# Performance work log

Measured on AMD Instinct MI355X. Metric: run time of the kernel, lower is better.

The kernel has to match this reference:

```python
import jax, jax.numpy as jnp
import numpy as np

B, T, D, H = 8, 2048, 512, 128

def setup_inputs() -> dict:
    key = jax.random.key(0)
    ks = jax.random.split(key, 8)
    s = lambda fan_in: 1.0 / np.sqrt(fan_in)
    return {
        "x": jax.random.normal(ks[0], (B, T, D), jnp.float32),
        "prediction": jax.random.normal(ks[1], (B, T, D), jnp.float32),
        "Wq": jax.random.uniform(ks[2], (D, H), jnp.float32, -s(D), s(D)),
        "bq": jnp.zeros((H,), jnp.float32),
        "Wk": jax.random.uniform(ks[3], (D, H), jnp.float32, -s(D), s(D)),
        "bk": jnp.zeros((H,), jnp.float32),
        "Wv": jax.random.uniform(ks[4], (D, D), jnp.float32, -s(D), s(D)),
        "bv": jnp.zeros((D,), jnp.float32),
        "Wf": jax.random.uniform(ks[5], (2 * D, D), jnp.float32, -s(2 * D), s(2 * D)),
        "bf": jnp.zeros((D,), jnp.float32),
    }

def reference(x, prediction, Wq, bq, Wk, bk, Wv, bv, Wf, bf):
    # q,k: [B,T,H]; v: [B,T,D]
    q = jnp.einsum('btd,dh->bth', prediction, Wq) + bq
    k = jnp.einsum('btd,dh->bth', x, Wk) + bk
    v = jnp.einsum('btd,de->bte', x, Wv) + bv
    # unscaled attention scores [B,T,T]
    scores = jnp.einsum('bth,bsh->bts', q, k)
    attn = jax.nn.softmax(scores, axis=-1)
    attended = jnp.einsum('bts,bsd->btd', attn, v)
    fusion_input = jnp.concatenate([prediction, attended], axis=-1)  # [B,T,2D]
    return jax.nn.sigmoid(jnp.einsum('btf,fd->btd', fusion_input, Wf) + bf)
```

## Files before the change

kernel.cpp:

```cpp
#include <hip/hip_runtime.h>
#include <hip/hip_bf16.h>


#define APF_B 8
#define APF_T 2048
#define APF_D 512
#define APF_H 128
#define APF_M (APF_B * APF_T)
#define FA_SB 64

typedef unsigned short u16;
typedef __attribute__((ext_vector_type(8))) short short8;
typedef __attribute__((ext_vector_type(4))) float f32x4;
typedef __attribute__((ext_vector_type(16))) float f32x16;

static __device__ __forceinline__ u16 f2bf(float x) {
    union { float f; unsigned int u; } cv;
    cv.f = x;
    unsigned int u = cv.u + 0x7FFFu + ((cv.u >> 16) & 1u);
    return (u16)(u >> 16);
}

static __device__ __forceinline__ void load16_lds(const u16* g, u16* l) {
    __builtin_amdgcn_global_load_lds(
        (const __attribute__((address_space(1))) unsigned int*)g,
        (__attribute__((address_space(3))) unsigned int*)l,
        16, 0, 0);
}

static __device__ __forceinline__ f32x16 zero16() {
    f32x16 v;
#pragma unroll
    for (int i = 0; i < 16; ++i) v[i] = 0.f;
    return v;
}


__global__ __launch_bounds__(256) void prep_all(
    const float* __restrict__ x,    u16* __restrict__ xb,
    const float* __restrict__ pred, u16* __restrict__ predb, long n4,
    const float* __restrict__ Wq, u16* __restrict__ WqT,
    const float* __restrict__ Wk, u16* __restrict__ WkT,
    const float* __restrict__ Wv, u16* __restrict__ WvT,
    const float* __restrict__ Wf, u16* __restrict__ WfT)
{
    const int bid = blockIdx.x;
    if (bid < 1024) {
        long i = bid * 256L + threadIdx.x;
        const long stride = 1024 * 256L;
        for (; i < 2 * n4; i += stride) {
            const float* in = (i < n4) ? x : pred;
            u16* out = (i < n4) ? xb : predb;
            const long j = (i < n4) ? i : (i - n4);
            const float4 v = ((const float4*)in)[j];
            ushort4 o;
            o.x = f2bf(v.x); o.y = f2bf(v.y); o.z = f2bf(v.z); o.w = f2bf(v.w);
            ((ushort4*)out)[j] = o;
        }
    } else {
        const long e = (bid - 1024) * 256L + threadIdx.x;
        if (e < 65536) {
            const long idx = e;
            const long n = idx / 512, k = idx % 512;
            WqT[idx] = f2bf(Wq[k * 128 + n]);
        } else if (e < 131072) {
            const long idx = e - 65536;
            const long n = idx / 512, k = idx % 512;
            WkT[idx] = f2bf(Wk[k * 128 + n]);
        } else if (e < 393216) {
            const long idx = e - 131072;
            const long n = idx / 512, k = idx % 512;
            WvT[idx] = f2bf(Wv[k * 512 + n]);
        } else if (e < 917504) {
            const long idx = e - 393216;
            const long n = idx / 1024, k = idx % 1024;
            WfT[idx] = f2bf(Wf[k * 512 + n]);
        }
    }
}

template <int DUAL, int EPI, int BIASM, int VBLK>
__global__ __launch_bounds__(256) void mfma_gemm(
    const u16* __restrict__ Ap, const u16* __restrict__ A2p, long lda,
    const u16* __restrict__ Bp, const u16* __restrict__ Bp2, long ldb,
    const float* __restrict__ biasp, const float* __restrict__ bias2,
    void* __restrict__ Cp, void* __restrict__ Cp2, long ldc, int K,
    long sA, long sB, long sC)
{
    __shared__ u16 smA[2][128 * 32];
    __shared__ u16 smB[2][128 * 32];

    const int tid  = threadIdx.x;
    const int lane = tid & 63;
    const int wid  = tid >> 6;
    const int wr   = wid >> 1;
    const int wc   = wid & 1;

    const long row0 = (long)blockIdx.y * 128;
    const long col0 = (long)blockIdx.x * 128;
    const long z    = blockIdx.z;

    const u16* Abase = (DUAL == 2) ? (z ? A2p : Ap) : (Ap + z * sA);
    const u16* Bbase = (DUAL == 2) ? (z ? Bp2 : Bp) : (Bp + z * sB);

    f32x4 acc[4][4];
#pragma unroll
    for (int i = 0; i < 4; ++i)
#pragma unroll
        for (int j = 0; j < 4; ++j)
            acc[i][j] = (f32x4){0.f, 0.f, 0.f, 0.f};

    const int lrow = (lane >> 4) * 4;
    const int lcol = lane & 15;
    const int q8   = (lane >> 4) * 8;

    auto stage = [&](int buf, int kb) {
#pragma unroll
        for (int rep = 0; rep < 2; ++rep) {
            const int c  = tid + rep * 256;
            const int r  = c >> 2;
            const int kc = (c & 3) * 8;
            const int wbase = (wid * 64 + rep * 256) * 8;
            const u16* ga;
            if (DUAL == 1 && (kb + kc) >= APF_D) {
                ga = A2p + (row0 + r) * lda + (kb + kc - APF_D);
            } else {
                ga = Abase + (row0 + r) * lda + (kb + kc);
            }
            load16_lds(ga, &smA[buf][wbase]);
            const u16* gb = Bbase + (col0 + r) * ldb + (kb + kc);
            load16_lds(gb, &smB[buf][wbase]);
        }
    };

    const int NT = K / 32;
    stage(0, 0);
    __syncthreads();
    int cur = 0;

    for (int t = 0; t < NT; ++t) {
        if (t + 1 < NT) stage(cur ^ 1, (t + 1) * 32);

        short8 av[4], bv4[4];
#pragma unroll
        for (int ti = 0; ti < 4; ++ti)
            av[ti] = *(const short8*)&smA[cur][(wr * 64 + ti * 16 + lcol) * 32 + q8];
#pragma unroll
        for (int tj = 0; tj < 4; ++tj)
            bv4[tj] = *(const short8*)&smB[cur][(wc * 64 + tj * 16 + lcol) * 32 + q8];

#pragma unroll
        for (int ti = 0; ti < 4; ++ti)
#pragma unroll
            for (int tj = 0; tj < 4; ++tj)
                acc[ti][tj] = __builtin_amdgcn_mfma_f32_16x16x32_bf16(
                    av[ti], bv4[tj], acc[ti][tj], 0, 0, 0);

        __syncthreads();
        cur ^= 1;
    }

    const float* bias = (DUAL == 2 && z) ? bias2 : biasp;

#pragma unroll
    for (int ti = 0; ti < 4; ++ti) {
        const long m0t = row0 + wr * 64 + ti * 16 + lrow;
#pragma unroll
        for (int tj = 0; tj < 4; ++tj) {
            const long n = col0 + wc * 64 + tj * 16 + lcol;
            const float bn = (BIASM == 0 && bias != nullptr) ? bias[n] : 0.f;
            if (EPI == 0) {
                u16* C = (u16*)((DUAL == 2 && z) ? Cp2 : Cp) + ((DUAL == 2) ? 0 : z * sC);
#pragma unroll
                for (int r = 0; r < 4; ++r) {
                    const long m = m0t + r;
                    const float bm = (BIASM == 1) ? bias[m] : bn;
                    long idx;
                    if (VBLK) {
                        idx = ((((m >> 5) * 256) + (n >> 3)) << 8) +
                              ((m & 31) << 3) + (n & 7);
                    } else {
                        idx = m * ldc + n;
                    }
                    C[idx] = f2bf(acc[ti][tj][r] + bm);
                }
            } else {
                float* C = (float*)Cp;
#pragma unroll
                for (int r = 0; r < 4; ++r) {
                    const float val = acc[ti][tj][r] + bn;
                    C[(m0t + r) * ldc + n] = 1.0f / (1.0f + expf(-val));
                }
            }
        }
    }
}

__global__ __launch_bounds__(256, 3) void attn_fused(
    const u16* __restrict__ qg, const u16* __restrict__ kg,
    const u16* __restrict__ vTg, u16* __restrict__ attg)
{
    __shared__ u16 sQ[64 * 128];
    __shared__ u16 sK[64 * 128];
    __shared__ u16 sP[64 * 64];
    __shared__ float sRS[192];

    const int tid  = threadIdx.x;
    const int lane = tid & 63;
    const int w    = tid >> 6;
    const int l31  = lane & 31;
    const int hi   = lane >> 5;
    const int qb   = w >> 1;
    const int sb   = w & 1;

    const int  bid = blockIdx.x;
    const long z   = bid & 7;
    const int  r   = bid >> 3;
    const long q0  = (long)(r & 31) * 64;
    const long d0  = (long)(r >> 5) * 256;

    const u16* kbase0 = kg + z * (long)APF_T * APF_H;

    {
        const u16* qsrc = qg + (z * APF_T + q0) * APF_H;
#pragma unroll
        for (int rep = 0; rep < 4; ++rep) {
            const int c    = tid + rep * 256;
            const int row  = c >> 4;
            const int col8 = (c & 15) * 8;
            load16_lds(qsrc + row * APF_H + (col8 ^ ((row & 15) << 3)), &sQ[c * 8]);
        }
#pragma unroll
        for (int rep = 0; rep < 4; ++rep) {
            const int c    = tid + rep * 256;
            const int row  = c >> 4;
            const int col8 = (c & 15) * 8;
            load16_lds(kbase0 + row * APF_H + (col8 ^ ((row & 15) << 3)), &sK[c * 8]);
        }
    }
    __syncthreads();

    f32x16 oacc[2][2];
#pragma unroll
    for (int i = 0; i < 2; ++i)
#pragma unroll
        for (int j = 0; j < 2; ++j) oacc[i][j] = zero16();
    f32x16 rsacc = zero16();

    const long dblk0 = (d0 >> 5) + w * 2;
    const u16* vzb = vTg + z * 1048576L + dblk0 * 65536L + (long)l31 * 8;

    const int qrow = qb * 32 + l31;
    const int krow = sb * 32 + l31;
    const int pcol = sb * 32 + l31;

    for (int kt = 0; kt < APF_T / FA_SB; ++kt) {
        f32x16 sacc = zero16();
#pragma unroll
        for (int ks = 0; ks < 8; ++ks) {
            const int colk = ks * 16 + hi * 8;
            const short8 av = *(const short8*)&sQ[qrow * 128 + (colk ^ ((qrow & 15) << 3))];
            const short8 bv = *(const short8*)&sK[krow * 128 + (colk ^ ((krow & 15) << 3))];
            sacc = __builtin_amdgcn_mfma_f32_32x32x16_bf16(av, bv, sacc, 0, 0, 0);
        }
        __syncthreads();

        if (kt + 1 < APF_T / FA_SB) {
            const u16* ksrc = kbase0 + (long)(kt + 1) * FA_SB * APF_H;
#pragma unroll
            for (int rep = 0; rep < 4; ++rep) {
                const int c    = tid + rep * 256;
                const int row  = c >> 4;
                const int col8 = (c & 15) * 8;
                load16_lds(ksrc + row * APF_H + (col8 ^ ((row & 15) << 3)), &sK[c * 8]);
            }
        }

        const long sbase = (long)kt * 8 + hi;
        short8 vf1[2][2];
#pragma unroll
        for (int dt = 0; dt < 2; ++dt)
#pragma unroll
            for (int ks = 0; ks < 2; ++ks)
                vf1[dt][ks] = *(const short8*)(vzb + dt * 65536L + (sbase + ks * 2) * 256);

#pragma unroll
        for (int rg = 0; rg < 16; ++rg) {
            const float e = __expf(sacc[rg]);
            rsacc[rg] += e;
            const int prow = qb * 32 + (rg & 3) + 8 * (rg >> 2) + 4 * hi;
            sP[prow * 64 + (pcol ^ ((prow & 7) << 3))] = f2bf(e);
        }
        __syncthreads();

#pragma unroll
        for (int ks = 0; ks < 2; ++ks) {
            const int colk = ks * 16 + hi * 8;
            short8 pa[2];
#pragma unroll
            for (int qt = 0; qt < 2; ++qt) {
                const int prow = qt * 32 + l31;
                pa[qt] = *(const short8*)&sP[prow * 64 + (colk ^ ((prow & 7) << 3))];
            }
#pragma unroll
            for (int dt = 0; dt < 2; ++dt)
#pragma unroll
                for (int qt = 0; qt < 2; ++qt)
                    oacc[qt][dt] = __builtin_amdgcn_mfma_f32_32x32x16_bf16(
                        pa[qt], vf1[dt][ks], oacc[qt][dt], 0, 0, 0);
        }

        short8 vf2[2][2];
#pragma unroll
        for (int dt = 0; dt < 2; ++dt)
#pragma unroll
            for (int ks = 0; ks < 2; ++ks)
                vf2[dt][ks] = *(const short8*)(vzb + dt * 65536L + (sbase + (ks + 2) * 2) * 256);

#pragma unroll
        for (int ks = 0; ks < 2; ++ks) {
            const int colk = (ks + 2) * 16 + hi * 8;
            short8 pa[2];
#pragma unroll
            for (int qt = 0; qt < 2; ++qt) {
                const int prow = qt * 32 + l31;
                pa[qt] = *(const short8*)&sP[prow * 64 + (colk ^ ((prow & 7) << 3))];
            }
#pragma unroll
            for (int dt = 0; dt < 2; ++dt)
#pragma unroll
                for (int qt = 0; qt < 2; ++qt)
                    oacc[qt][dt] = __builtin_amdgcn_mfma_f32_32x32x16_bf16(
                        pa[qt], vf2[dt][ks], oacc[qt][dt], 0, 0, 0);
        }
    }

#pragma unroll
    for (int rg = 0; rg < 16; ++rg) {
        float s = rsacc[rg];
        s += __shfl_xor(s, 1);
        s += __shfl_xor(s, 2);
        s += __shfl_xor(s, 4);
        s += __shfl_xor(s, 8);
        s += __shfl_xor(s, 16);
        rsacc[rg] = s;
    }
    if (l31 == 0) {
#pragma unroll
        for (int rg = 0; rg < 16; ++rg) {
            const int row = (rg & 3) + 8 * (rg >> 2) + 4 * hi;
            sRS[w * 32 + row] = rsacc[rg];
        }
    }
    __syncthreads();
    if (tid < 64) {
        const int qb2 = tid >> 5, r2 = tid & 31;
        sRS[128 + tid] = 1.0f / (sRS[(qb2 * 2 + 0) * 32 + r2] +
                                 sRS[(qb2 * 2 + 1) * 32 + r2]);
    }
    __syncthreads();

    const long rowg0 = z * APF_T + q0;
    const long colg0 = d0 + (long)w * 64;
#pragma unroll
    for (int qt = 0; qt < 2; ++qt)
#pragma unroll
        for (int rg = 0; rg < 16; ++rg) {
            const int row = qt * 32 + (rg & 3) + 8 * (rg >> 2) + 4 * hi;
            const float inv = sRS[128 + row];
#pragma unroll
            for (int dt = 0; dt < 2; ++dt)
                attg[(rowg0 + row) * APF_D + colg0 + dt * 32 + l31] =
                    f2bf(oacc[qt][dt][rg] * inv);
        }
}

extern "C" void kernel_launch(void* const* d_in, const int* in_sizes, int n_in,
                              void* d_out, int out_size, void* d_ws, size_t ws_size,
                              hipStream_t stream)
{
    (void)in_sizes; (void)n_in; (void)out_size; (void)ws_size;

    const float* x    = (const float*)d_in[0];
    const float* pred = (const float*)d_in[1];
    const float* Wq   = (const float*)d_in[2];
    const float* bq   = (const float*)d_in[3];
    const float* Wk   = (const float*)d_in[4];
    const float* bk   = (const float*)d_in[5];
    const float* Wv   = (const float*)d_in[6];
    const float* bv   = (const float*)d_in[7];
    const float* Wf   = (const float*)d_in[8];
    const float* bfu  = (const float*)d_in[9];

    u16* wsp   = (u16*)d_ws;
    u16* xb    = wsp;
    u16* predb = xb    + (long)APF_M * APF_D;
    u16* qb    = predb + (long)APF_M * APF_D;
    u16* kbuf  = qb    + (long)APF_M * APF_H;
    u16* vTb   = kbuf  + (long)APF_M * APF_H;
    u16* attb  = vTb   + (long)APF_M * APF_D;
    u16* WqT   = attb  + (long)APF_M * APF_D;
    u16* WkT   = WqT   + (long)APF_H * APF_D;
    u16* WvT   = WkT   + (long)APF_H * APF_D;
    u16* WfT   = WvT   + (long)APF_D * APF_D;

    const dim3 thr(256);
    const long nBTD4 = (long)APF_M * APF_D / 4;

    prep_all<<<dim3(1024 + 3584), thr, 0, stream>>>(
        x, xb, pred, predb, nBTD4, Wq, WqT, Wk, WkT, Wv, WvT, Wf, WfT);

    mfma_gemm<2, 0, 0, 0><<<dim3(1, 128, 2), thr, 0, stream>>>(
        predb, xb, APF_D, WqT, WkT, APF_D, bq, bk, qb, kbuf, APF_H, APF_D,
        0, 0, 0);

    mfma_gemm<0, 0, 1, 1><<<dim3(16, 4, 8), thr, 0, stream>>>(
        WvT, nullptr, APF_D, xb, nullptr, APF_D, bv, nullptr, vTb, nullptr,
        APF_T, APF_D, 0, (long)APF_T * APF_D, (long)APF_D * APF_T);

    attn_fused<<<dim3(512), thr, 0, stream>>>(qb, kbuf, vTb, attb);

    mfma_gemm<1, 2, 0, 0><<<dim3(4, 128, 1), thr, 0, stream>>>(
        predb, attb, APF_D, WfT, nullptr, 2 * APF_D, bfu, nullptr, d_out, nullptr,
        APF_D, 2 * APF_D, 0, 0, 0);
}
```

Baseline: 262.7 us.

## Split attention output columns finer and keep Q fragments in registers

Each attention block now produces 128 output columns instead of 256, doubling the grid to 1024 blocks. Q fragments are loaded directly into registers instead of LDS, and each wave holds half the output accumulators. This aims to raise occupancy and fill more CUs, but it doubles the redundant QK^T score and exp computation across column splits.

```diff
diff --git a/kernel.cpp b/kernel.cpp
--- a/kernel.cpp
+++ b/kernel.cpp
@@ -200,7 +200,6 @@
     const u16* __restrict__ qg, const u16* __restrict__ kg,
     const u16* __restrict__ vTg, u16* __restrict__ attg)
 {
-    __shared__ u16 sQ[64 * 128];
     __shared__ u16 sK[64 * 128];
     __shared__ u16 sP[64 * 64];
     __shared__ float sRS[192];
@@ -217,40 +216,34 @@
     const long z   = bid & 7;
     const int  r   = bid >> 3;
     const long q0  = (long)(r & 31) * 64;
-    const long d0  = (long)(r >> 5) * 256;
+    const long d0  = (long)(r >> 5) * 128;
 
     const u16* kbase0 = kg + z * (long)APF_T * APF_H;
 
+#pragma unroll
+    for (int rep = 0; rep < 4; ++rep) {
+        const int c    = tid + rep * 256;
+        const int row  = c >> 4;
+        const int col8 = (c & 15) * 8;
+        load16_lds(kbase0 + row * APF_H + (col8 ^ ((row & 15) << 3)), &sK[c * 8]);
+    }
+
+    short8 qf[8];
     {
-        const u16* qsrc = qg + (z * APF_T + q0) * APF_H;
-#pragma unroll
-        for (int rep = 0; rep < 4; ++rep) {
-            const int c    = tid + rep * 256;
-            const int row  = c >> 4;
-            const int col8 = (c & 15) * 8;
-            load16_lds(qsrc + row * APF_H + (col8 ^ ((row & 15) << 3)), &sQ[c * 8]);
-        }
-#pragma unroll
-        for (int rep = 0; rep < 4; ++rep) {
-            const int c    = tid + rep * 256;
-            const int row  = c >> 4;
-            const int col8 = (c & 15) * 8;
-            load16_lds(kbase0 + row * APF_H + (col8 ^ ((row & 15) << 3)), &sK[c * 8]);
-        }
+        const u16* qsrc = qg + (z * APF_T + q0 + qb * 32 + l31) * APF_H;
+#pragma unroll
+        for (int ks = 0; ks < 8; ++ks)
+            qf[ks] = *(const short8*)(qsrc + ks * 16 + hi * 8);
     }
     __syncthreads();
 
-    f32x16 oacc[2][2];
-#pragma unroll
-    for (int i = 0; i < 2; ++i)
-#pragma unroll
-        for (int j = 0; j < 2; ++j) oacc[i][j] = zero16();
+    f32x16 oacc[2];
+    oacc[0] = zero16(); oacc[1] = zero16();
     f32x16 rsacc = zero16();
 
-    const long dblk0 = (d0 >> 5) + w * 2;
+    const long dblk0 = (d0 >> 5) + w;
     const u16* vzb = vTg + z * 1048576L + dblk0 * 65536L + (long)l31 * 8;
 
-    const int qrow = qb * 32 + l31;
     const int krow = sb * 32 + l31;
     const int pcol = sb * 32 + l31;
 
@@ -259,9 +252,8 @@
 #pragma unroll
         for (int ks = 0; ks < 8; ++ks) {
             const int colk = ks * 16 + hi * 8;
-            const short8 av = *(const short8*)&sQ[qrow * 128 + (colk ^ ((qrow & 15) << 3))];
             const short8 bv = *(const short8*)&sK[krow * 128 + (colk ^ ((krow & 15) << 3))];
-            sacc = __builtin_amdgcn_mfma_f32_32x32x16_bf16(av, bv, sacc, 0, 0, 0);
+            sacc = __builtin_amdgcn_mfma_f32_32x32x16_bf16(qf[ks], bv, sacc, 0, 0, 0);
         }
         __syncthreads();
 
@@ -277,12 +269,10 @@
         }
 
         const long sbase = (long)kt * 8 + hi;
-        short8 vf1[2][2];
-#pragma unroll
-        for (int dt = 0; dt < 2; ++dt)
-#pragma unroll
-            for (int ks = 0; ks < 2; ++ks)
-                vf1[dt][ks] = *(const short8*)(vzb + dt * 65536L + (sbase + ks * 2) * 256);
+        short8 vf[4];
+#pragma unroll
+        for (int ks = 0; ks < 4; ++ks)
+            vf[ks] = *(const short8*)(vzb + (sbase + ks * 2) * 256);
 
 #pragma unroll
         for (int rg = 0; rg < 16; ++rg) {
@@ -294,7 +284,7 @@
         __syncthreads();
 
 #pragma unroll
-        for (int ks = 0; ks < 2; ++ks) {
+        for (int ks = 0; ks < 4; ++ks) {
             const int colk = ks * 16 + hi * 8;
             short8 pa[2];
 #pragma unroll
@@ -303,35 +293,9 @@
                 pa[qt] = *(const short8*)&sP[prow * 64 + (colk ^ ((prow & 7) << 3))];
             }
 #pragma unroll
-            for (int dt = 0; dt < 2; ++dt)
-#pragma unroll
-                for (int qt = 0; qt < 2; ++qt)
-                    oacc[qt][dt] = __builtin_amdgcn_mfma_f32_32x32x16_bf16(
-                        pa[qt], vf1[dt][ks], oacc[qt][dt], 0, 0, 0);
-        }
-
-        short8 vf2[2][2];
-#pragma unroll
-        for (int dt = 0; dt < 2; ++dt)
-#pragma unroll
-            for (int ks = 0; ks < 2; ++ks)
-                vf2[dt][ks] = *(const short8*)(vzb + dt * 65536L + (sbase + (ks + 2) * 2) * 256);
-
-#pragma unroll
-        for (int ks = 0; ks < 2; ++ks) {
-            const int colk = (ks + 2) * 16 + hi * 8;
-            short8 pa[2];
-#pragma unroll
-            for (int qt = 0; qt < 2; ++qt) {
-                const int prow = qt * 32 + l31;
-                pa[qt] = *(const short8*)&sP[prow * 64 + (colk ^ ((prow & 7) << 3))];
-            }
-#pragma unroll
-            for (int dt = 0; dt < 2; ++dt)
-#pragma unroll
-                for (int qt = 0; qt < 2; ++qt)
-                    oacc[qt][dt] = __builtin_amdgcn_mfma_f32_32x32x16_bf16(
-                        pa[qt], vf2[dt][ks], oacc[qt][dt], 0, 0, 0);
+            for (int qt = 0; qt < 2; ++qt)
+                oacc[qt] = __builtin_amdgcn_mfma_f32_32x32x16_bf16(
+                    pa[qt], vf[ks], oacc[qt], 0, 0, 0);
         }
     }
 
@@ -361,17 +325,14 @@
     __syncthreads();
 
     const long rowg0 = z * APF_T + q0;
-    const long colg0 = d0 + (long)w * 64;
+    const long colg  = d0 + (long)w * 32 + l31;
 #pragma unroll
     for (int qt = 0; qt < 2; ++qt)
 #pragma unroll
         for (int rg = 0; rg < 16; ++rg) {
             const int row = qt * 32 + (rg & 3) + 8 * (rg >> 2) + 4 * hi;
-            const float inv = sRS[128 + row];
-#pragma unroll
-            for (int dt = 0; dt < 2; ++dt)
-                attg[(rowg0 + row) * APF_D + colg0 + dt * 32 + l31] =
-                    f2bf(oacc[qt][dt][rg] * inv);
+            attg[(rowg0 + row) * APF_D + colg] =
+                f2bf(oacc[qt][rg] * sRS[128 + row]);
         }
 }
 
@@ -418,7 +379,7 @@
         WvT, nullptr, APF_D, xb, nullptr, APF_D, bv, nullptr, vTb, nullptr,
         APF_T, APF_D, 0, (long)APF_T * APF_D, (long)APF_D * APF_T);
 
-    attn_fused<<<dim3(512), thr, 0, stream>>>(qb, kbuf, vTb, attb);
+    attn_fused<<<dim3(1024), thr, 0, stream>>>(qb, kbuf, vTb, attb);
 
     mfma_gemm<1, 2, 0, 0><<<dim3(4, 128, 1), thr, 0, stream>>>(
         predb, attb, APF_D, WfT, nullptr, 2 * APF_D, bfu, nullptr, d_out, nullptr,
```

After: 290.4 us. 10.6% more time.

## Fuse fp32-to-bf16 activation conversion into GEMM loaders and merge Q/K/V GEMMs

Applied to the files above, without the earlier changes.

The separate pass that converted x and prediction to bf16 is removed. GEMMs now load fp32 activations into registers, convert them and write bf16 into LDS, while weights still arrive through direct-to-LDS DMA. The Q/K and V projection GEMMs are merged into one launch, which removes a kernel launch and the round trip of the bf16 activation copies through memory. In exchange the GEMM inner loop does conversion ALU work, reads twice the bytes per activation element, and the x tile is reconverted by every block that reads it.

```diff
diff --git a/kernel.cpp b/kernel.cpp
--- a/kernel.cpp
+++ b/kernel.cpp
@@ -7,7 +7,7 @@
 #define APF_D 512
 #define APF_H 128
 #define APF_M (APF_B * APF_T)
-#define FA_SB 64
+#define FA_SB 128
 
 typedef unsigned short u16;
 typedef __attribute__((ext_vector_type(8))) short short8;
@@ -36,73 +36,46 @@
 }
 
 
-__global__ __launch_bounds__(256) void prep_all(
-    const float* __restrict__ x,    u16* __restrict__ xb,
-    const float* __restrict__ pred, u16* __restrict__ predb, long n4,
+__global__ __launch_bounds__(256) void prep_w(
     const float* __restrict__ Wq, u16* __restrict__ WqT,
     const float* __restrict__ Wk, u16* __restrict__ WkT,
     const float* __restrict__ Wv, u16* __restrict__ WvT,
     const float* __restrict__ Wf, u16* __restrict__ WfT)
 {
-    const int bid = blockIdx.x;
-    if (bid < 1024) {
-        long i = bid * 256L + threadIdx.x;
-        const long stride = 1024 * 256L;
-        for (; i < 2 * n4; i += stride) {
-            const float* in = (i < n4) ? x : pred;
-            u16* out = (i < n4) ? xb : predb;
-            const long j = (i < n4) ? i : (i - n4);
-            const float4 v = ((const float4*)in)[j];
-            ushort4 o;
-            o.x = f2bf(v.x); o.y = f2bf(v.y); o.z = f2bf(v.z); o.w = f2bf(v.w);
-            ((ushort4*)out)[j] = o;
-        }
-    } else {
-        const long e = (bid - 1024) * 256L + threadIdx.x;
-        if (e < 65536) {
-            const long idx = e;
-            const long n = idx / 512, k = idx % 512;
-            WqT[idx] = f2bf(Wq[k * 128 + n]);
-        } else if (e < 131072) {
-            const long idx = e - 65536;
-            const long n = idx / 512, k = idx % 512;
-            WkT[idx] = f2bf(Wk[k * 128 + n]);
-        } else if (e < 393216) {
-            const long idx = e - 131072;
-            const long n = idx / 512, k = idx % 512;
-            WvT[idx] = f2bf(Wv[k * 512 + n]);
-        } else if (e < 917504) {
-            const long idx = e - 393216;
-            const long n = idx / 1024, k = idx % 1024;
-            WfT[idx] = f2bf(Wf[k * 512 + n]);
-        }
-    }
-}
-
-template <int DUAL, int EPI, int BIASM, int VBLK>
-__global__ __launch_bounds__(256) void mfma_gemm(
-    const u16* __restrict__ Ap, const u16* __restrict__ A2p, long lda,
-    const u16* __restrict__ Bp, const u16* __restrict__ Bp2, long ldb,
-    const float* __restrict__ biasp, const float* __restrict__ bias2,
-    void* __restrict__ Cp, void* __restrict__ Cp2, long ldc, int K,
-    long sA, long sB, long sC)
-{
-    __shared__ u16 smA[2][128 * 32];
-    __shared__ u16 smB[2][128 * 32];
-
+    const long e = blockIdx.x * 256L + threadIdx.x;
+    if (e < 65536) {
+        const long idx = e;
+        const long n = idx / 512, k = idx % 512;
+        WqT[idx] = f2bf(Wq[k * 128 + n]);
+    } else if (e < 131072) {
+        const long idx = e - 65536;
+        const long n = idx / 512, k = idx % 512;
+        WkT[idx] = f2bf(Wk[k * 128 + n]);
+    } else if (e < 393216) {
+        const long idx = e - 131072;
+        const long n = idx / 512, k = idx % 512;
+        WvT[idx] = f2bf(Wv[k * 512 + n]);
+    } else if (e < 917504) {
+        const long idx = e - 393216;
+        const long n = idx / 1024, k = idx % 1024;
+        WfT[idx] = f2bf(Wf[k * 512 + n]);
+    }
+}
+
+template <int ADT, int BDT, int EPI, int BIASM, int VBLK>
+static __device__ __forceinline__ void gemm_body(
+    u16 (&smA)[2][4096], u16 (&smB)[2][4096],
+    const void* Ap, const void* A2p, long lda,
+    const void* Bp, long ldb,
+    const float* bias, void* Cp, long ldc, int K,
+    long row0, long col0)
+{
     const int tid  = threadIdx.x;
     const int lane = tid & 63;
     const int wid  = tid >> 6;
     const int wr   = wid >> 1;
     const int wc   = wid & 1;
 
-    const long row0 = (long)blockIdx.y * 128;
-    const long col0 = (long)blockIdx.x * 128;
-    const long z    = blockIdx.z;
-
-    const u16* Abase = (DUAL == 2) ? (z ? A2p : Ap) : (Ap + z * sA);
-    const u16* Bbase = (DUAL == 2) ? (z ? Bp2 : Bp) : (Bp + z * sB);
-
     f32x4 acc[4][4];
 #pragma unroll
     for (int i = 0; i < 4; ++i)
@@ -114,32 +87,98 @@
     const int lcol = lane & 15;
     const int q8   = (lane >> 4) * 8;
 
-    auto stage = [&](int buf, int kb) {
-#pragma unroll
-        for (int rep = 0; rep < 2; ++rep) {
-            const int c  = tid + rep * 256;
-            const int r  = c >> 2;
-            const int kc = (c & 3) * 8;
-            const int wbase = (wid * 64 + rep * 256) * 8;
-            const u16* ga;
-            if (DUAL == 1 && (kb + kc) >= APF_D) {
-                ga = A2p + (row0 + r) * lda + (kb + kc - APF_D);
-            } else {
-                ga = Abase + (row0 + r) * lda + (kb + kc);
-            }
-            load16_lds(ga, &smA[buf][wbase]);
-            const u16* gb = Bbase + (col0 + r) * ldb + (kb + kc);
-            load16_lds(gb, &smB[buf][wbase]);
+    float4 ra[2][2], rb[2][2];
+
+    auto loadA = [&](int kb) {
+        if (ADT == 1 || (ADT == 2 && kb < APF_D)) {
+            const float* Af = (const float*)Ap;
+#pragma unroll
+            for (int rep = 0; rep < 2; ++rep) {
+                const int c = tid + rep * 256;
+                const int rr = c >> 2, kc = (c & 3) * 8;
+                const float* ga = Af + (row0 + rr) * lda + kb + kc;
+                ra[rep][0] = *(const float4*)ga;
+                ra[rep][1] = *(const float4*)(ga + 4);
+            }
+        }
+    };
+    auto loadB = [&](int kb) {
+        if (BDT == 1) {
+            const float* Bf = (const float*)Bp;
+#pragma unroll
+            for (int rep = 0; rep < 2; ++rep) {
+                const int c = tid + rep * 256;
+                const int rr = c >> 2, kc = (c & 3) * 8;
+                const float* gb = Bf + (col0 + rr) * ldb + kb + kc;
+                rb[rep][0] = *(const float4*)gb;
+                rb[rep][1] = *(const float4*)(gb + 4);
+            }
+        }
+    };
+    auto dmaA = [&](int buf, int kb) {
+        if (ADT == 0 || (ADT == 2 && kb >= APF_D)) {
+            const u16* Ab = (ADT == 2) ? (const u16*)A2p : (const u16*)Ap;
+            const int kk = (ADT == 2) ? kb - APF_D : kb;
+            const long ld = (ADT == 2) ? APF_D : lda;
+#pragma unroll
+            for (int rep = 0; rep < 2; ++rep) {
+                const int c = tid + rep * 256;
+                const int rr = c >> 2, kc = (c & 3) * 8;
+                const int wbase = (wid * 64 + rep * 256) * 8;
+                load16_lds(Ab + (row0 + rr) * ld + kk + kc, &smA[buf][wbase]);
+            }
+        }
+    };
+    auto dmaB = [&](int buf, int kb) {
+        if (BDT == 0) {
+            const u16* Bb = (const u16*)Bp;
+#pragma unroll
+            for (int rep = 0; rep < 2; ++rep) {
+                const int c = tid + rep * 256;
+                const int rr = c >> 2, kc = (c & 3) * 8;
+                const int wbase = (wid * 64 + rep * 256) * 8;
+                load16_lds(Bb + (col0 + rr) * ldb + kb + kc, &smB[buf][wbase]);
+            }
+        }
+    };
+    auto cvt8 = [&](const float4& a, const float4& b) {
+        short8 v;
+        v[0] = (short)f2bf(a.x); v[1] = (short)f2bf(a.y);
+        v[2] = (short)f2bf(a.z); v[3] = (short)f2bf(a.w);
+        v[4] = (short)f2bf(b.x); v[5] = (short)f2bf(b.y);
+        v[6] = (short)f2bf(b.z); v[7] = (short)f2bf(b.w);
+        return v;
+    };
+    auto writeA = [&](int buf, int kb) {
+        if (ADT == 1 || (ADT == 2 && kb < APF_D)) {
+#pragma unroll
+            for (int rep = 0; rep < 2; ++rep) {
+                const int c = tid + rep * 256;
+                *(short8*)&smA[buf][c * 8] = cvt8(ra[rep][0], ra[rep][1]);
+            }
+        }
+    };
+    auto writeB = [&](int buf, int kb) {
+        if (BDT == 1) {
+#pragma unroll
+            for (int rep = 0; rep < 2; ++rep) {
+                const int c = tid + rep * 256;
+                *(short8*)&smB[buf][c * 8] = cvt8(rb[rep][0], rb[rep][1]);
+            }
         }
     };
 
     const int NT = K / 32;
-    stage(0, 0);
-    __syncthreads();
+    loadA(0); loadB(0);
+    writeA(0, 0); writeB(0, 0);
+    dmaA(0, 0); dmaB(0, 0);
+
     int cur = 0;
-
     for (int t = 0; t < NT; ++t) {
-        if (t + 1 < NT) stage(cur ^ 1, (t + 1) * 32);
+        const int kb2 = (t + 1) * 32;
+        if (t + 1 < NT) { loadA(kb2); loadB(kb2); }
+        __syncthreads();
+        if (t + 1 < NT) { dmaA(cur ^ 1, kb2); dmaB(cur ^ 1, kb2); }
 
         short8 av[4], bv4[4];
 #pragma unroll
@@ -156,11 +195,9 @@
                 acc[ti][tj] = __builtin_amdgcn_mfma_f32_16x16x32_bf16(
                     av[ti], bv4[tj], acc[ti][tj], 0, 0, 0);
 
-        __syncthreads();
+        if (t + 1 < NT) { writeA(cur ^ 1, kb2); writeB(cur ^ 1, kb2); }
         cur ^= 1;
     }
-
-    const float* bias = (DUAL == 2 && z) ? bias2 : biasp;
 
 #pragma unroll
     for (int ti = 0; ti < 4; ++ti) {
@@ -168,9 +205,9 @@
 #pragma unroll
         for (int tj = 0; tj < 4; ++tj) {
             const long n = col0 + wc * 64 + tj * 16 + lcol;
-            const float bn = (BIASM == 0 && bias != nullptr) ? bias[n] : 0.f;
+            const float bn = (BIASM == 0) ? bias[n] : 0.f;
             if (EPI == 0) {
-                u16* C = (u16*)((DUAL == 2 && z) ? Cp2 : Cp) + ((DUAL == 2) ? 0 : z * sC);
+                u16* C = (u16*)Cp;
 #pragma unroll
                 for (int r = 0; r < 4; ++r) {
                     const long m = m0t + r;
@@ -196,6 +233,51 @@
     }
 }
 
+__global__ __launch_bounds__(256, 3) void mid_gemms(
+    const float* __restrict__ x, const float* __restrict__ pred,
+    const u16* __restrict__ WqT, const u16* __restrict__ WkT,
+    const u16* __restrict__ WvT,
+    const float* __restrict__ bq, const float* __restrict__ bk,
+    const float* __restrict__ bv,
+    u16* __restrict__ qb, u16* __restrict__ kbuf, u16* __restrict__ vTb)
+{
+    __shared__ u16 smA[2][4096];
+    __shared__ u16 smB[2][4096];
+
+    const int bid = blockIdx.x;
+    if (bid < 256) {
+        const int zz = bid >> 7, by = bid & 127;
+        gemm_body<1, 0, 0, 0, 0>(smA, smB,
+            zz ? (const void*)x : (const void*)pred, nullptr, APF_D,
+            zz ? WkT : WqT, APF_D,
+            zz ? bk : bq, zz ? (void*)kbuf : (void*)qb, APF_H, APF_D,
+            (long)by * 128, 0);
+    } else {
+        const int t = bid - 256;
+        const int zz = t >> 6, rem = t & 63;
+        const int bx = rem & 15, by = rem >> 4;
+        gemm_body<0, 1, 0, 1, 1>(smA, smB,
+            WvT, nullptr, APF_D,
+            (const void*)(x + (long)zz * APF_T * APF_D), APF_D,
+            bv, (void*)(vTb + (long)zz * 1048576L), APF_T, APF_D,
+            (long)by * 128, (long)bx * 128);
+    }
+}
+
+__global__ __launch_bounds__(256, 2) void fusion_gemm(
+    const float* __restrict__ pred, const u16* __restrict__ attb,
+    const u16* __restrict__ WfT, const float* __restrict__ bfu,
+    float* __restrict__ out)
+{
+    __shared__ u16 smA[2][4096];
+    __shared__ u16 smB[2][4096];
+    gemm_body<2, 0, 2, 0, 0>(smA, smB,
+        (const void*)pred, (const void*)attb, APF_D,
+        WfT, 2 * APF_D,
+        bfu, (void*)out, APF_D, 2 * APF_D,
+        (long)blockIdx.y * 128, (long)blockIdx.x * 128);
+}
+
 __global__ __launch_bounds__(256, 3) void attn_fused(
     const u16* __restrict__ qg, const u16* __restrict__ kg,
     const u16* __restrict__ vTg, u16* __restrict__ attg)
@@ -254,7 +336,7 @@
     const int krow = sb * 32 + l31;
     const int pcol = sb * 32 + l31;
 
-    for (int kt = 0; kt < APF_T / FA_SB; ++kt) {
+    for (int kt = 0; kt < APF_T / 64; ++kt) {
         f32x16 sacc = zero16();
 #pragma unroll
         for (int ks = 0; ks < 8; ++ks) {
@@ -265,8 +347,8 @@
         }
         __syncthreads();
 
-        if (kt + 1 < APF_T / FA_SB) {
-            const u16* ksrc = kbase0 + (long)(kt + 1) * FA_SB * APF_H;
+        if (kt + 1 < APF_T / 64) {
+            const u16* ksrc = kbase0 + (long)(kt + 1) * 64 * APF_H;
 #pragma unroll
             for (int rep = 0; rep < 4; ++rep) {
                 const int c    = tid + rep * 256;
@@ -392,35 +474,25 @@
     const float* Wf   = (const float*)d_in[8];
     const float* bfu  = (const float*)d_in[9];
 
-    u16* wsp   = (u16*)d_ws;
-    u16* xb    = wsp;
-    u16* predb = xb    + (long)APF_M * APF_D;
-    u16* qb    = predb + (long)APF_M * APF_D;
-    u16* kbuf  = qb    + (long)APF_M * APF_H;
-    u16* vTb   = kbuf  + (long)APF_M * APF_H;
-    u16* attb  = vTb   + (long)APF_M * APF_D;
-    u16* WqT   = attb  + (long)APF_M * APF_D;
-    u16* WkT   = WqT   + (long)APF_H * APF_D;
-    u16* WvT   = WkT   + (long)APF_H * APF_D;
-    u16* WfT   = WvT   + (long)APF_D * APF_D;
+    u16* wsp  = (u16*)d_ws;
+    u16* qb   = wsp;
+    u16* kbuf = qb   + (long)APF_M * APF_H;
+    u16* vTb  = kbuf + (long)APF_M * APF_H;
+    u16* attb = vTb  + (long)APF_M * APF_D;
+    u16* WqT  = attb + (long)APF_M * APF_D;
+    u16* WkT  = WqT  + (long)APF_H * APF_D;
+    u16* WvT  = WkT  + (long)APF_H * APF_D;
+    u16* WfT  = WvT  + (long)APF_D * APF_D;
 
     const dim3 thr(256);
-    const long nBTD4 = (long)APF_M * APF_D / 4;
-
-    prep_all<<<dim3(1024 + 3584), thr, 0, stream>>>(
-        x, xb, pred, predb, nBTD4, Wq, WqT, Wk, WkT, Wv, WvT, Wf, WfT);
-
-    mfma_gemm<2, 0, 0, 0><<<dim3(1, 128, 2), thr, 0, stream>>>(
-        predb, xb, APF_D, WqT, WkT, APF_D, bq, bk, qb, kbuf, APF_H, APF_D,
-        0, 0, 0);
-
-    mfma_gemm<0, 0, 1, 1><<<dim3(16, 4, 8), thr, 0, stream>>>(
-        WvT, nullptr, APF_D, xb, nullptr, APF_D, bv, nullptr, vTb, nullptr,
-        APF_T, APF_D, 0, (long)APF_T * APF_D, (long)APF_D * APF_T);
+
+    prep_w<<<dim3(3584), thr, 0, stream>>>(Wq, WqT, Wk, WkT, Wv, WvT, Wf, WfT);
+
+    mid_gemms<<<dim3(768), thr, 0, stream>>>(
+        x, pred, WqT, WkT, WvT, bq, bk, bv, qb, kbuf, vTb);
 
     attn_fused<<<dim3(512), thr, 0, stream>>>(qb, kbuf, vTb, attb);
 
-    mfma_gemm<1, 2, 0, 0><<<dim3(4, 128, 1), thr, 0, stream>>>(
-        predb, attb, APF_D, WfT, nullptr, 2 * APF_D, bfu, nullptr, d_out, nullptr,
-        APF_D, 2 * APF_D, 0, 0, 0);
-}
+    fusion_gemm<<<dim3(4, 128), thr, 0, stream>>>(pred, attb, WfT, bfu,
+                                                  (float*)d_out);
+}
```

New measurement: 254.0 us. 3.3% less time.
